# Optimization experiments

Measured on AMD Instinct MI355X. Metric: run time of the kernel, lower is better.

Reference implementation:

```python
import jax, jax.numpy as jnp
import numpy as np

N = 100000
E = 3200000
D_IN = 83
D_HID = 1024
N_CLASSES = 25


def setup_inputs() -> dict:
    key = jax.random.key(0)
    ks = jax.random.split(key, 10)
    feature = jax.random.normal(ks[0], (N, D_IN), dtype=jnp.float32)
    edge_row = jax.random.randint(ks[1], (E,), 0, N, dtype=jnp.int32)
    edge_col = jax.random.randint(ks[2], (E,), 0, N, dtype=jnp.int32)
    adj_val = jax.random.uniform(ks[3], (E,), dtype=jnp.float32)
    # Conv1d(1 -> 4, kernel 5, pad 2): weight [out=4, in=1, k=5]
    conv_w = jax.random.normal(ks[4], (4, 1, 5), dtype=jnp.float32) * 0.2
    conv_b = jnp.zeros((4,), dtype=jnp.float32)
    # GCN weights (kaiming-uniform-like scale), zero biases
    W1 = jax.random.uniform(ks[5], (D_IN, D_HID), dtype=jnp.float32,
                            minval=-1.0, maxval=1.0) * np.sqrt(6.0 / D_IN)
    b1 = jnp.zeros((D_HID,), dtype=jnp.float32)
    W2 = jax.random.uniform(ks[6], (D_HID, N_CLASSES), dtype=jnp.float32,
                            minval=-1.0, maxval=1.0) * np.sqrt(6.0 / D_HID)
    b2 = jnp.zeros((N_CLASSES,), dtype=jnp.float32)
    return {"feature": feature, "conv_w": conv_w, "conv_b": conv_b,
            "W1": W1, "b1": b1, "W2": W2, "b2": b2,
            "adj_val": adj_val, "edge_row": edge_row, "edge_col": edge_col}


def _spmm(vals, row, col, X):
    # sparse(adj) @ X : gather source rows, scale by edge value, scatter-add to dest
    return jax.ops.segment_sum(vals[:, None] * X[col], row, num_segments=N)


def reference(feature, conv_w, conv_b, W1, b1, W2, b2, adj_val, edge_row, edge_col):
    # Conv1d prelude: [N,1,83] -> [N,4,83], sum over channels, relu -> [N,83]
    x = jax.lax.conv_general_dilated(
        feature[:, None, :], conv_w, window_strides=(1,), padding=[(2, 2)],
        dimension_numbers=("NCH", "OIH", "NCH"))
    x = x + conv_b[None, :, None]
    x = jax.nn.relu(jnp.sum(x, axis=1))
    # GCN layer 1: relu(A @ (x W1) + b1)
    h = jax.nn.relu(_spmm(adj_val, edge_row, edge_col, x @ W1) + b1)
    # GCN layer 2: A @ (h W2) + b2
    logits = _spmm(adj_val, edge_row, edge_col, h @ W2) + b2
    return logits
```

## Files before the change

### kernel.cpp

```cpp
#include <hip/hip_runtime.h>

#define NN   100000
#define EE   3200000
#define DIN  83
#define DHID 1024
#define NCLS 25
#define XPAD 96
#define ZPAD 32

#define NBK     391
#define CHUNK   8192

typedef __attribute__((__ext_vector_type__(8))) short sh8;
typedef __attribute__((__ext_vector_type__(4))) float f4_t;

static __device__ __forceinline__ float relu_(float v) { return v > 0.f ? v : 0.f; }

static __device__ __forceinline__ unsigned short f2bf(float f) {
  unsigned int u = __float_as_uint(f);
  unsigned int r = u + 0x7FFFu + ((u >> 16) & 1u);
  return (unsigned short)(r >> 16);
}
static __device__ __forceinline__ float bflo(unsigned int q) {
  return __uint_as_float(q << 16);
}
static __device__ __forceinline__ float bfhi(unsigned int q) {
  return __uint_as_float(q & 0xFFFF0000u);
}

__global__ void conv_relu_k(const float* __restrict__ feature,
                            const float* __restrict__ conv_w,
                            const float* __restrict__ conv_b,
                            unsigned short* __restrict__ x) {
  float ws0 = conv_w[0] + conv_w[5] + conv_w[10] + conv_w[15];
  float ws1 = conv_w[1] + conv_w[6] + conv_w[11] + conv_w[16];
  float ws2 = conv_w[2] + conv_w[7] + conv_w[12] + conv_w[17];
  float ws3 = conv_w[3] + conv_w[8] + conv_w[13] + conv_w[18];
  float ws4 = conv_w[4] + conv_w[9] + conv_w[14] + conv_w[19];
  float bs  = conv_b[0] + conv_b[1] + conv_b[2] + conv_b[3];
  const int total = NN * XPAD;
  for (int idx = blockIdx.x * blockDim.x + threadIdx.x; idx < total;
       idx += gridDim.x * blockDim.x) {
    int n = idx / XPAD;
    int i = idx - n * XPAD;
    unsigned short o = 0;
    if (i < DIN) {
      const float* f = feature + (size_t)n * DIN;
      float acc = bs;
      if (i >= 2)      acc += ws0 * f[i - 2];
      if (i >= 1)      acc += ws1 * f[i - 1];
      acc += ws2 * f[i];
      if (i + 1 < DIN) acc += ws3 * f[i + 1];
      if (i + 2 < DIN) acc += ws4 * f[i + 2];
      o = f2bf(relu_(acc));
    }
    x[idx] = o;
  }
}

__global__ void prep_k(const float* __restrict__ W1, unsigned short* __restrict__ w1t,
                       const float* __restrict__ W2, unsigned short* __restrict__ w2t,
                       int* __restrict__ gbk) {
  int idx = blockIdx.x * blockDim.x + threadIdx.x;
  if (idx < DHID * XPAD) {
    int k = idx / DHID;
    int n = idx - k * DHID;
    float v = (k < DIN) ? W1[k * DHID + n] : 0.f;
    w1t[n * XPAD + k] = f2bf(v);
  }
  if (idx < 32 * DHID) {
    int k = idx / 32;
    int n = idx - k * 32;
    float v = (n < NCLS) ? W2[k * NCLS + n] : 0.f;
    w2t[n * DHID + k] = f2bf(v);
  }
  if (idx < NBK * 16) gbk[idx] = 0;
}


__global__ __launch_bounds__(512) void bucket_hist_k(
    const int* __restrict__ row, int* __restrict__ gbk) {
  __shared__ int cnt[NBK];
  const int tid = threadIdx.x;
  for (int b = tid; b < NBK; b += 512) cnt[b] = 0;
  __syncthreads();
  const int cb = blockIdx.x * CHUNK;
  const int csize = (cb + CHUNK <= EE) ? CHUNK : (EE - cb);
  for (int i = tid; i < csize; i += 512)
    atomicAdd(&cnt[row[cb + i] >> 8], 1);
  __syncthreads();
  for (int b = tid; b < NBK; b += 512)
    if (cnt[b]) atomicAdd(&gbk[b * 16], cnt[b]);
}

__global__ void scan_buckets_k(const int* __restrict__ gbk,
                               int* __restrict__ bbase, int* __restrict__ gcur) {
  __shared__ int sd[512];
  int t = threadIdx.x;
  int v = (t < NBK) ? gbk[t * 16] : 0;
  sd[t] = v;
  __syncthreads();
  for (int off = 1; off < 512; off <<= 1) {
    int add = (t >= off) ? sd[t - off] : 0;
    __syncthreads();
    sd[t] += add;
    __syncthreads();
  }
  if (t < NBK) {
    int excl = sd[t] - v;
    bbase[t] = excl;
    gcur[t * 16] = excl;
  }
  if (t == 0) bbase[NBK] = EE;
}

__global__ __launch_bounds__(256) void partition_k(
    const float* __restrict__ vals, const int* __restrict__ row,
    const int* __restrict__ col, int* __restrict__ gcur,
    int2* __restrict__ tmp) {
  __shared__ int cnt[NBK];
  __shared__ int lcur[NBK];
  const int tid = threadIdx.x;
  const int cb = blockIdx.x * CHUNK;
  const int csize = (cb + CHUNK <= EE) ? CHUNK : (EE - cb);

  for (int b = tid; b < NBK; b += 256) cnt[b] = 0;
  __syncthreads();
  for (int i = tid; i < csize; i += 256)
    atomicAdd(&cnt[row[cb + i] >> 8], 1);
  __syncthreads();
  for (int b = tid; b < NBK; b += 256)
    lcur[b] = cnt[b] ? atomicAdd(&gcur[b * 16], cnt[b]) : 0;
  __syncthreads();
  for (int i = tid; i < csize; i += 256) {
    int r = row[cb + i];
    int pos = atomicAdd(&lcur[r >> 8], 1);
    tmp[pos] = make_int2(col[cb + i] | ((r & 255) << 17),
                         __float_as_int(vals[cb + i]));
  }
}

__global__ __launch_bounds__(512) void fine_scatter2_k(
    const int* __restrict__ bbase, const int2* __restrict__ tmp,
    int2* __restrict__ csr, int* __restrict__ offs, int* __restrict__ counts) {
  __shared__ int cnt[256];
  __shared__ int sd[256];
  __shared__ int lcur[256];
  const int tid = threadIdx.x;
  const int b = blockIdx.x;
  const int r0 = b * 256;
  const int gstart = bbase[b];
  const int nedge = bbase[b + 1] - gstart;
  if (tid < 256) cnt[tid] = 0;
  __syncthreads();
  for (int i = tid; i < nedge; i += 512)
    atomicAdd(&cnt[((unsigned)tmp[gstart + i].x) >> 17], 1);
  __syncthreads();
  int v = 0;
  if (tid < 256) { v = cnt[tid]; sd[tid] = v; }
  __syncthreads();
  for (int off = 1; off < 256; off <<= 1) {
    int add = (tid >= off && tid < 256) ? sd[tid - off] : 0;
    __syncthreads();
    if (tid < 256) sd[tid] += add;
    __syncthreads();
  }
  if (tid < 256) {
    int excl = gstart + sd[tid] - v;
    int r = r0 + tid;
    if (r < NN) {
      offs[r] = excl;
      counts[r] = v;
    }
    lcur[tid] = excl;
  }
  __syncthreads();
  for (int i = tid; i < nedge; i += 512) {
    int2 p = tmp[gstart + i];
    int rl = ((unsigned)p.x) >> 17;
    int pos = atomicAdd(&lcur[rl], 1);
    csr[pos] = make_int2(p.x & 0x1FFFF, p.y);
  }
}

__global__ __launch_bounds__(256) void spmm83_g(
    const int* __restrict__ offs, const int* __restrict__ cnt,
    const int2* __restrict__ csr, const unsigned short* __restrict__ x,
    unsigned short* __restrict__ ax) {
  int wave = (int)((blockIdx.x * blockDim.x + threadIdx.x) >> 6);
  int lane = threadIdx.x & 63;
  if (wave >= NN) return;
  int s = __builtin_amdgcn_readfirstlane(offs[wave]);
  int n = __builtin_amdgcn_readfirstlane(cnt[wave]);
  const bool act = lane < 48;
  const int d2 = lane * 2;
  float a0 = 0.f, a1 = 0.f;
  int i = 0;
  for (; i + 8 <= n; i += 8) {
    int2 p[8];
#pragma unroll
    for (int u = 0; u < 8; ++u) p[u] = csr[s + i + u];
    if (act) {
      unsigned int q[8];
#pragma unroll
      for (int u = 0; u < 8; ++u)
        q[u] = *(const unsigned int*)&x[(size_t)p[u].x * XPAD + d2];
#pragma unroll
      for (int u = 0; u < 8; ++u) {
        float v = __int_as_float(p[u].y);
        a0 += v * bflo(q[u]);
        a1 += v * bfhi(q[u]);
      }
    }
  }
  for (; i < n; ++i) {
    int2 p = csr[s + i];
    if (act) {
      unsigned int q = *(const unsigned int*)&x[(size_t)p.x * XPAD + d2];
      float v = __int_as_float(p.y);
      a0 += v * bflo(q);
      a1 += v * bfhi(q);
    }
  }
  if (act) {
    unsigned int o = (unsigned int)f2bf(a0) | ((unsigned int)f2bf(a1) << 16);
    *(unsigned int*)&ax[(size_t)wave * XPAD + d2] = o;
  }
}

__global__ __launch_bounds__(256) void spmm25_g(
    const int* __restrict__ offs, const int* __restrict__ cnt,
    const int2* __restrict__ csr, const unsigned short* __restrict__ zb,
    const float* __restrict__ b2, float* __restrict__ out) {
  int gw = (int)((blockIdx.x * blockDim.x + threadIdx.x) >> 6);
  int lane = threadIdx.x & 63;
  int sub = lane >> 4;
  int d2 = (lane & 15) * 2;
  int r = gw * 4 + sub;
  if (r >= NN) return;
  int s = offs[r];
  int n = cnt[r];
  float a0 = 0.f, a1 = 0.f;
  int i = 0;
  for (; i + 4 <= n; i += 4) {
    int2 p0 = csr[s + i + 0];
    int2 p1 = csr[s + i + 1];
    int2 p2 = csr[s + i + 2];
    int2 p3 = csr[s + i + 3];
    unsigned int q0 = *(const unsigned int*)&zb[(size_t)p0.x * ZPAD + d2];
    unsigned int q1 = *(const unsigned int*)&zb[(size_t)p1.x * ZPAD + d2];
    unsigned int q2 = *(const unsigned int*)&zb[(size_t)p2.x * ZPAD + d2];
    unsigned int q3 = *(const unsigned int*)&zb[(size_t)p3.x * ZPAD + d2];
    float v0 = __int_as_float(p0.y), v1 = __int_as_float(p1.y);
    float v2 = __int_as_float(p2.y), v3 = __int_as_float(p3.y);
    a0 += v0 * bflo(q0) + v1 * bflo(q1) + v2 * bflo(q2) + v3 * bflo(q3);
    a1 += v0 * bfhi(q0) + v1 * bfhi(q1) + v2 * bfhi(q2) + v3 * bfhi(q3);
  }
  for (; i < n; ++i) {
    int2 p = csr[s + i];
    unsigned int q = *(const unsigned int*)&zb[(size_t)p.x * ZPAD + d2];
    float v = __int_as_float(p.y);
    a0 += v * bflo(q);
    a1 += v * bfhi(q);
  }
  if (d2 < NCLS)     out[(size_t)r * NCLS + d2]     = a0 + b2[d2];
  if (d2 + 1 < NCLS) out[(size_t)r * NCLS + d2 + 1] = a1 + b2[d2 + 1];
}

__global__ __launch_bounds__(256) void fused_mlp_mfma(
    const unsigned short* __restrict__ axg, const unsigned short* __restrict__ w1t,
    const float* __restrict__ b1, const unsigned short* __restrict__ w2t,
    unsigned short* __restrict__ zb) {
  __shared__ __align__(16) unsigned short axs[128 * 104];
  __shared__ __align__(16) unsigned short hs[128 * 136];
  __shared__ float b1s[DHID];
  const int tid = threadIdx.x;
  const int n0 = blockIdx.x * 128;

  for (int idx = tid; idx < 128 * 12; idx += 256) {
    int m = idx / 12;
    int c8 = idx - m * 12;
    int node = n0 + m;
    sh8 v = {0, 0, 0, 0, 0, 0, 0, 0};
    if (node < NN) v = *(const sh8*)&axg[(size_t)node * XPAD + c8 * 8];
    *(sh8*)&axs[m * 104 + c8 * 8] = v;
  }
  for (int i = tid; i < DHID; i += 256) b1s[i] = b1[i];
  __syncthreads();

  const int lane = tid & 63;
  const int w = tid >> 6;
  const int quad = lane >> 4;
  const int tn = lane & 15;
  const int mta = w;
  const int mtb = w + 4;

  sh8 a1[8][3];
#pragma unroll
  for (int mt = 0; mt < 8; ++mt)
#pragma unroll
    for (int kc = 0; kc < 3; ++kc)
      a1[mt][kc] = *(const sh8*)&axs[(mt * 16 + tn) * 104 + kc * 32 + quad * 8];

  f4_t za0 = {0.f, 0.f, 0.f, 0.f}, za1 = {0.f, 0.f, 0.f, 0.f};
  f4_t zb0 = {0.f, 0.f, 0.f, 0.f}, zb1 = {0.f, 0.f, 0.f, 0.f};

  for (int c = 0; c < 8; ++c) {
    const int cb = c * 128;
#pragma unroll
    for (int nti = 0; nti < 2; ++nti) {
      const int nt = w * 2 + nti;
      const int ng = cb + nt * 16 + tn;
      const unsigned short* wr = &w1t[(size_t)ng * XPAD + quad * 8];
      sh8 b0 = *(const sh8*)&wr[0];
      sh8 b1f = *(const sh8*)&wr[32];
      sh8 b2f = *(const sh8*)&wr[64];
      float bias = b1s[ng];
#pragma unroll
      for (int mt = 0; mt < 8; ++mt) {
        f4_t acc = {0.f, 0.f, 0.f, 0.f};
        acc = __builtin_amdgcn_mfma_f32_16x16x32_bf16(a1[mt][0], b0, acc, 0, 0, 0);
        acc = __builtin_amdgcn_mfma_f32_16x16x32_bf16(a1[mt][1], b1f, acc, 0, 0, 0);
        acc = __builtin_amdgcn_mfma_f32_16x16x32_bf16(a1[mt][2], b2f, acc, 0, 0, 0);
#pragma unroll
        for (int r = 0; r < 4; ++r) {
          float v = relu_(acc[r] + bias);
          hs[(mt * 16 + quad * 4 + r) * 136 + nt * 16 + tn] = f2bf(v);
        }
      }
    }
    __syncthreads();
#pragma unroll
    for (int kc = 0; kc < 4; ++kc) {
      sh8 bl = *(const sh8*)&w2t[(size_t)tn * DHID + cb + kc * 32 + quad * 8];
      sh8 bh = *(const sh8*)&w2t[(size_t)(16 + tn) * DHID + cb + kc * 32 + quad * 8];
      sh8 aa = *(const sh8*)&hs[(mta * 16 + tn) * 136 + kc * 32 + quad * 8];
      za0 = __builtin_amdgcn_mfma_f32_16x16x32_bf16(aa, bl, za0, 0, 0, 0);
      za1 = __builtin_amdgcn_mfma_f32_16x16x32_bf16(aa, bh, za1, 0, 0, 0);
      sh8 ab = *(const sh8*)&hs[(mtb * 16 + tn) * 136 + kc * 32 + quad * 8];
      zb0 = __builtin_amdgcn_mfma_f32_16x16x32_bf16(ab, bl, zb0, 0, 0, 0);
      zb1 = __builtin_amdgcn_mfma_f32_16x16x32_bf16(ab, bh, zb1, 0, 0, 0);
    }
    __syncthreads();
  }

#pragma unroll
  for (int r = 0; r < 4; ++r) {
    int na = n0 + mta * 16 + quad * 4 + r;
    if (na < NN) {
      zb[(size_t)na * ZPAD + tn]      = f2bf(za0[r]);
      zb[(size_t)na * ZPAD + 16 + tn] = f2bf(za1[r]);
    }
    int nb = n0 + mtb * 16 + quad * 4 + r;
    if (nb < NN) {
      zb[(size_t)nb * ZPAD + tn]      = f2bf(zb0[r]);
      zb[(size_t)nb * ZPAD + 16 + tn] = f2bf(zb1[r]);
    }
  }
}

extern "C" void kernel_launch(void* const* d_in, const int* in_sizes, int n_in,
                              void* d_out, int out_size, void* d_ws, size_t ws_size,
                              hipStream_t stream) {
  const float* feature = (const float*)d_in[0];
  const float* conv_w  = (const float*)d_in[1];
  const float* conv_b  = (const float*)d_in[2];
  const float* W1      = (const float*)d_in[3];
  const float* b1      = (const float*)d_in[4];
  const float* W2      = (const float*)d_in[5];
  const float* b2      = (const float*)d_in[6];
  const float* adj     = (const float*)d_in[7];
  const int*   erow    = (const int*)d_in[8];
  const int*   ecol    = (const int*)d_in[9];
  float* out = (float*)d_out;

  char* B = (char*)d_ws;
  size_t o = 0;
  auto alloc = [&](size_t bytes, size_t align) -> void* {
    o = (o + align - 1) & ~(align - 1);
    void* p = B + o;
    o += bytes;
    return p;
  };
  unsigned short* x    = (unsigned short*)alloc((size_t)NN * XPAD * 2, 16);
  unsigned short* ax   = (unsigned short*)alloc((size_t)NN * XPAD * 2, 16);
  unsigned short* zb   = (unsigned short*)alloc((size_t)NN * ZPAD * 2, 16);
  int*   counts  = (int*)alloc((size_t)NN * 4, 16);
  int*   offs    = (int*)alloc((size_t)NN * 4, 16);
  int*   gcur    = (int*)alloc((size_t)NBK * 16 * 4, 64);
  int*   gbk     = (int*)alloc((size_t)NBK * 16 * 4, 64);
  int*   bbase   = (int*)alloc((size_t)(NBK + 1) * 4, 16);
  unsigned short* w1t = (unsigned short*)alloc((size_t)DHID * XPAD * 2, 16);
  unsigned short* w2t = (unsigned short*)alloc((size_t)32 * DHID * 2, 16);
  int2*  tmp     = (int2*)alloc((size_t)EE * 8, 16);
  int2*  csr     = (int2*)alloc((size_t)EE * 8, 16);

  conv_relu_k<<<8192, 256, 0, stream>>>(feature, conv_w, conv_b, x);
  prep_k<<<(DHID * XPAD + 255) / 256, 256, 0, stream>>>(W1, w1t, W2, w2t, gbk);
  bucket_hist_k<<<(EE + CHUNK - 1) / CHUNK, 512, 0, stream>>>(erow, gbk);
  scan_buckets_k<<<1, 512, 0, stream>>>(gbk, bbase, gcur);
  partition_k<<<(EE + CHUNK - 1) / CHUNK, 256, 0, stream>>>(adj, erow, ecol, gcur, tmp);
  fine_scatter2_k<<<NBK, 512, 0, stream>>>(bbase, tmp, csr, offs, counts);
  spmm83_g<<<(NN + 3) / 4, 256, 0, stream>>>(offs, counts, csr, x, ax);
  fused_mlp_mfma<<<(NN + 127) / 128, 256, 0, stream>>>(ax, w1t, b1, w2t, zb);
  spmm25_g<<<(NN + 15) / 16, 256, 0, stream>>>(offs, counts, csr, zb, b2, out);
}
```

Before: 483.7 us.

## Sort edges by source-column phase within row groups to improve gather locality

```diff
diff --git a/kernel.cpp b/kernel.cpp
--- a/kernel.cpp
+++ b/kernel.cpp
@@ -10,6 +10,11 @@
 
 #define NBK     391
 #define CHUNK   8192
+
+#define CB      13
+#define NP      13
+#define NKEY    (NP * 256)
+#define NWAVE   (NN / 16)
 
 typedef __attribute__((__ext_vector_type__(8))) short sh8;
 typedef __attribute__((__ext_vector_type__(4))) float f4_t;
@@ -140,131 +145,199 @@
   }
 }
 
-__global__ __launch_bounds__(512) void fine_scatter2_k(
+__global__ __launch_bounds__(512) void fine_scatter3_k(
     const int* __restrict__ bbase, const int2* __restrict__ tmp,
-    int2* __restrict__ csr, int* __restrict__ offs, int* __restrict__ counts) {
-  __shared__ int cnt[256];
-  __shared__ int sd[256];
-  __shared__ int lcur[256];
+    int2* __restrict__ csr2, int* __restrict__ off3) {
+  __shared__ int cnt[3584];
+  __shared__ int lcur[3584];
+  __shared__ int sd[512];
   const int tid = threadIdx.x;
   const int b = blockIdx.x;
-  const int r0 = b * 256;
   const int gstart = bbase[b];
   const int nedge = bbase[b + 1] - gstart;
-  if (tid < 256) cnt[tid] = 0;
-  __syncthreads();
-  for (int i = tid; i < nedge; i += 512)
-    atomicAdd(&cnt[((unsigned)tmp[gstart + i].x) >> 17], 1);
-  __syncthreads();
-  int v = 0;
-  if (tid < 256) { v = cnt[tid]; sd[tid] = v; }
-  __syncthreads();
-  for (int off = 1; off < 256; off <<= 1) {
-    int add = (tid >= off && tid < 256) ? sd[tid - off] : 0;
-    __syncthreads();
-    if (tid < 256) sd[tid] += add;
-    __syncthreads();
-  }
-  if (tid < 256) {
-    int excl = gstart + sd[tid] - v;
-    int r = r0 + tid;
-    if (r < NN) {
-      offs[r] = excl;
-      counts[r] = v;
-    }
-    lcur[tid] = excl;
-  }
+  for (int k = tid; k < 3584; k += 512) cnt[k] = 0;
+  __syncthreads();
+  for (int i = tid; i < nedge; i += 512) {
+    int px = tmp[gstart + i].x;
+    int key = ((px & 0x1FFFF) >> CB) * 256 + (int)(((unsigned)px) >> 17);
+    atomicAdd(&cnt[key], 1);
+  }
+  __syncthreads();
+  int v[7];
+  int run = 0;
+#pragma unroll
+  for (int j = 0; j < 7; ++j) { v[j] = cnt[tid * 7 + j]; run += v[j]; }
+  sd[tid] = run;
+  __syncthreads();
+  for (int off = 1; off < 512; off <<= 1) {
+    int add = (tid >= off) ? sd[tid - off] : 0;
+    __syncthreads();
+    sd[tid] += add;
+    __syncthreads();
+  }
+  int base = gstart + sd[tid] - run;
+#pragma unroll
+  for (int j = 0; j < 7; ++j) { cnt[tid * 7 + j] = base; base += v[j]; }
+  __syncthreads();
+  for (int k = tid; k < 3584; k += 512) lcur[k] = cnt[k];
+  for (int k = tid; k < NKEY; k += 512) off3[b * NKEY + k] = cnt[k];
+  if (b == NBK - 1 && tid == 0) off3[NBK * NKEY] = EE;
   __syncthreads();
   for (int i = tid; i < nedge; i += 512) {
     int2 p = tmp[gstart + i];
-    int rl = ((unsigned)p.x) >> 17;
-    int pos = atomicAdd(&lcur[rl], 1);
-    csr[pos] = make_int2(p.x & 0x1FFFF, p.y);
-  }
-}
-
-__global__ __launch_bounds__(256) void spmm83_g(
-    const int* __restrict__ offs, const int* __restrict__ cnt,
-    const int2* __restrict__ csr, const unsigned short* __restrict__ x,
-    unsigned short* __restrict__ ax) {
-  int wave = (int)((blockIdx.x * blockDim.x + threadIdx.x) >> 6);
-  int lane = threadIdx.x & 63;
-  if (wave >= NN) return;
-  int s = __builtin_amdgcn_readfirstlane(offs[wave]);
-  int n = __builtin_amdgcn_readfirstlane(cnt[wave]);
+    int rloc = (int)(((unsigned)p.x) >> 17);
+    int key = ((p.x & 0x1FFFF) >> CB) * 256 + rloc;
+    int pos = atomicAdd(&lcur[key], 1);
+    csr2[pos] = make_int2((p.x & 0x1FFFF) | ((rloc & 15) << 17), p.y);
+  }
+}
+
+#define FLUSH16(SCUR, C0, C1)                              \
+  switch (SCUR) {                                          \
+    case 0:  a0[0]  += (C0); a1[0]  += (C1); break;        \
+    case 1:  a0[1]  += (C0); a1[1]  += (C1); break;        \
+    case 2:  a0[2]  += (C0); a1[2]  += (C1); break;        \
+    case 3:  a0[3]  += (C0); a1[3]  += (C1); break;        \
+    case 4:  a0[4]  += (C0); a1[4]  += (C1); break;        \
+    case 5:  a0[5]  += (C0); a1[5]  += (C1); break;        \
+    case 6:  a0[6]  += (C0); a1[6]  += (C1); break;        \
+    case 7:  a0[7]  += (C0); a1[7]  += (C1); break;        \
+    case 8:  a0[8]  += (C0); a1[8]  += (C1); break;        \
+    case 9:  a0[9]  += (C0); a1[9]  += (C1); break;        \
+    case 10: a0[10] += (C0); a1[10] += (C1); break;        \
+    case 11: a0[11] += (C0); a1[11] += (C1); break;        \
+    case 12: a0[12] += (C0); a1[12] += (C1); break;        \
+    case 13: a0[13] += (C0); a1[13] += (C1); break;        \
+    case 14: a0[14] += (C0); a1[14] += (C1); break;        \
+    case 15: a0[15] += (C0); a1[15] += (C1); break;        \
+    default: break;                                        \
+  }
+
+__global__ __launch_bounds__(512, 8) void spmm83_p(
+    const int* __restrict__ off3, const int2* __restrict__ csr2,
+    const unsigned short* __restrict__ x, unsigned short* __restrict__ ax) {
+  const int gw = (int)((blockIdx.x * 512 + threadIdx.x) >> 6);
+  const int lane = threadIdx.x & 63;
+  if (gw >= NWAVE) return;
+  const int b = gw >> 4;
+  const int g0 = (gw & 15) << 4;
   const bool act = lane < 48;
   const int d2 = lane * 2;
-  float a0 = 0.f, a1 = 0.f;
-  int i = 0;
-  for (; i + 8 <= n; i += 8) {
-    int2 p[8];
-#pragma unroll
-    for (int u = 0; u < 8; ++u) p[u] = csr[s + i + u];
-    if (act) {
-      unsigned int q[8];
-#pragma unroll
-      for (int u = 0; u < 8; ++u)
-        q[u] = *(const unsigned int*)&x[(size_t)p[u].x * XPAD + d2];
-#pragma unroll
-      for (int u = 0; u < 8; ++u) {
-        float v = __int_as_float(p[u].y);
-        a0 += v * bflo(q[u]);
-        a1 += v * bfhi(q[u]);
-      }
-    }
-  }
-  for (; i < n; ++i) {
-    int2 p = csr[s + i];
-    if (act) {
-      unsigned int q = *(const unsigned int*)&x[(size_t)p.x * XPAD + d2];
-      float v = __int_as_float(p.y);
-      a0 += v * bflo(q);
-      a1 += v * bfhi(q);
-    }
-  }
+  float a0[16], a1[16];
+#pragma unroll
+  for (int k = 0; k < 16; ++k) { a0[k] = 0.f; a1[k] = 0.f; }
+
+  for (int p = 0; p < NP; ++p) {
+    const int kb = b * NKEY + p * 256 + g0;
+    const int s = __builtin_amdgcn_readfirstlane(off3[kb]);
+    const int e = __builtin_amdgcn_readfirstlane(off3[kb + 16]);
+    int scur = 0;
+    float c0 = 0.f, c1 = 0.f;
+    int i = s;
+    for (; i + 4 <= e; i += 4) {
+      int2 p4[4];
+#pragma unroll
+      for (int u = 0; u < 4; ++u) p4[u] = csr2[i + u];
+      unsigned q[4];
+      if (act) {
+#pragma unroll
+        for (int u = 0; u < 4; ++u)
+          q[u] = *(const unsigned*)&x[(size_t)(p4[u].x & 0x1FFFF) * XPAD + d2];
+      }
+#pragma unroll
+      for (int u = 0; u < 4; ++u) {
+        int srl = __builtin_amdgcn_readfirstlane((int)(((unsigned)p4[u].x) >> 17));
+        if (srl != scur) {
+          FLUSH16(scur, c0, c1);
+          scur = srl; c0 = 0.f; c1 = 0.f;
+        }
+        float v = __int_as_float(p4[u].y);
+        c0 += v * bflo(q[u]);
+        c1 += v * bfhi(q[u]);
+      }
+    }
+    for (; i < e; ++i) {
+      int2 pe = csr2[i];
+      unsigned q = 0;
+      if (act) q = *(const unsigned*)&x[(size_t)(pe.x & 0x1FFFF) * XPAD + d2];
+      int srl = __builtin_amdgcn_readfirstlane((int)(((unsigned)pe.x) >> 17));
+      if (srl != scur) {
+        FLUSH16(scur, c0, c1);
+        scur = srl; c0 = 0.f; c1 = 0.f;
+      }
+      float v = __int_as_float(pe.y);
+      c0 += v * bflo(q);
+      c1 += v * bfhi(q);
+    }
+    FLUSH16(scur, c0, c1);
+  }
+
   if (act) {
-    unsigned int o = (unsigned int)f2bf(a0) | ((unsigned int)f2bf(a1) << 16);
-    *(unsigned int*)&ax[(size_t)wave * XPAD + d2] = o;
-  }
-}
-
-__global__ __launch_bounds__(256) void spmm25_g(
-    const int* __restrict__ offs, const int* __restrict__ cnt,
-    const int2* __restrict__ csr, const unsigned short* __restrict__ zb,
-    const float* __restrict__ b2, float* __restrict__ out) {
-  int gw = (int)((blockIdx.x * blockDim.x + threadIdx.x) >> 6);
-  int lane = threadIdx.x & 63;
-  int sub = lane >> 4;
-  int d2 = (lane & 15) * 2;
-  int r = gw * 4 + sub;
-  if (r >= NN) return;
-  int s = offs[r];
-  int n = cnt[r];
-  float a0 = 0.f, a1 = 0.f;
-  int i = 0;
-  for (; i + 4 <= n; i += 4) {
-    int2 p0 = csr[s + i + 0];
-    int2 p1 = csr[s + i + 1];
-    int2 p2 = csr[s + i + 2];
-    int2 p3 = csr[s + i + 3];
-    unsigned int q0 = *(const unsigned int*)&zb[(size_t)p0.x * ZPAD + d2];
-    unsigned int q1 = *(const unsigned int*)&zb[(size_t)p1.x * ZPAD + d2];
-    unsigned int q2 = *(const unsigned int*)&zb[(size_t)p2.x * ZPAD + d2];
-    unsigned int q3 = *(const unsigned int*)&zb[(size_t)p3.x * ZPAD + d2];
-    float v0 = __int_as_float(p0.y), v1 = __int_as_float(p1.y);
-    float v2 = __int_as_float(p2.y), v3 = __int_as_float(p3.y);
-    a0 += v0 * bflo(q0) + v1 * bflo(q1) + v2 * bflo(q2) + v3 * bflo(q3);
-    a1 += v0 * bfhi(q0) + v1 * bfhi(q1) + v2 * bfhi(q2) + v3 * bfhi(q3);
-  }
-  for (; i < n; ++i) {
-    int2 p = csr[s + i];
-    unsigned int q = *(const unsigned int*)&zb[(size_t)p.x * ZPAD + d2];
-    float v = __int_as_float(p.y);
-    a0 += v * bflo(q);
-    a1 += v * bfhi(q);
-  }
-  if (d2 < NCLS)     out[(size_t)r * NCLS + d2]     = a0 + b2[d2];
-  if (d2 + 1 < NCLS) out[(size_t)r * NCLS + d2 + 1] = a1 + b2[d2 + 1];
+    const int r0 = gw << 4;
+#pragma unroll
+    for (int k = 0; k < 16; ++k) {
+      unsigned o = (unsigned)f2bf(a0[k]) | ((unsigned)f2bf(a1[k]) << 16);
+      *(unsigned*)&ax[(size_t)(r0 + k) * XPAD + d2] = o;
+    }
+  }
+}
+
+__global__ __launch_bounds__(512, 8) void spmm25_p(
+    const int* __restrict__ off3, const int2* __restrict__ csr2,
+    const unsigned short* __restrict__ zbt, const float* __restrict__ b2,
+    float* __restrict__ out) {
+  const int gw = (int)((blockIdx.x * 512 + threadIdx.x) >> 6);
+  const int lane = threadIdx.x & 63;
+  if (gw >= NWAVE) return;
+  const int b = gw >> 4;
+  const int g0 = (gw & 15) << 4;
+  const int grp = lane >> 4;
+  const int d2 = (lane & 15) * 2;
+  float acc0[4], acc1[4];
+#pragma unroll
+  for (int s = 0; s < 4; ++s) { acc0[s] = 0.f; acc1[s] = 0.f; }
+
+  for (int p = 0; p < NP; ++p) {
+    const int kb = b * NKEY + p * 256 + g0;
+#pragma unroll
+    for (int s = 0; s < 4; ++s) {
+      const int st = __builtin_amdgcn_readfirstlane(off3[kb + s * 4]);
+      const int en = __builtin_amdgcn_readfirstlane(off3[kb + s * 4 + 4]);
+      const int myrl = s * 4 + grp;
+      float t0 = acc0[s], t1 = acc1[s];
+      int i = st;
+      for (; i + 4 <= en; i += 4) {
+        int2 p4[4];
+#pragma unroll
+        for (int u = 0; u < 4; ++u) p4[u] = csr2[i + u];
+#pragma unroll
+        for (int u = 0; u < 4; ++u) {
+          unsigned q = *(const unsigned*)&zbt[(size_t)(p4[u].x & 0x1FFFF) * ZPAD + d2];
+          int rl = (int)(((unsigned)p4[u].x) >> 17);
+          float v = (rl == myrl) ? __int_as_float(p4[u].y) : 0.f;
+          t0 += v * bflo(q);
+          t1 += v * bfhi(q);
+        }
+      }
+      for (; i < en; ++i) {
+        int2 pe = csr2[i];
+        unsigned q = *(const unsigned*)&zbt[(size_t)(pe.x & 0x1FFFF) * ZPAD + d2];
+        int rl = (int)(((unsigned)pe.x) >> 17);
+        float v = (rl == myrl) ? __int_as_float(pe.y) : 0.f;
+        t0 += v * bflo(q);
+        t1 += v * bfhi(q);
+      }
+      acc0[s] = t0; acc1[s] = t1;
+    }
+  }
+
+  const int r0 = gw << 4;
+#pragma unroll
+  for (int s = 0; s < 4; ++s) {
+    int r = r0 + s * 4 + grp;
+    if (d2 < NCLS)     out[(size_t)r * NCLS + d2]     = acc0[s] + b2[d2];
+    if (d2 + 1 < NCLS) out[(size_t)r * NCLS + d2 + 1] = acc1[s] + b2[d2 + 1];
+  }
 }
 
 __global__ __launch_bounds__(256) void fused_mlp_mfma(
@@ -385,23 +458,22 @@
   unsigned short* x    = (unsigned short*)alloc((size_t)NN * XPAD * 2, 16);
   unsigned short* ax   = (unsigned short*)alloc((size_t)NN * XPAD * 2, 16);
   unsigned short* zb   = (unsigned short*)alloc((size_t)NN * ZPAD * 2, 16);
-  int*   counts  = (int*)alloc((size_t)NN * 4, 16);
-  int*   offs    = (int*)alloc((size_t)NN * 4, 16);
   int*   gcur    = (int*)alloc((size_t)NBK * 16 * 4, 64);
   int*   gbk     = (int*)alloc((size_t)NBK * 16 * 4, 64);
   int*   bbase   = (int*)alloc((size_t)(NBK + 1) * 4, 16);
+  int*   off3    = (int*)alloc(((size_t)NBK * NKEY + 1) * 4, 16);
   unsigned short* w1t = (unsigned short*)alloc((size_t)DHID * XPAD * 2, 16);
   unsigned short* w2t = (unsigned short*)alloc((size_t)32 * DHID * 2, 16);
   int2*  tmp     = (int2*)alloc((size_t)EE * 8, 16);
-  int2*  csr     = (int2*)alloc((size_t)EE * 8, 16);
+  int2*  csr2    = (int2*)alloc((size_t)EE * 8, 16);
 
   conv_relu_k<<<8192, 256, 0, stream>>>(feature, conv_w, conv_b, x);
   prep_k<<<(DHID * XPAD + 255) / 256, 256, 0, stream>>>(W1, w1t, W2, w2t, gbk);
   bucket_hist_k<<<(EE + CHUNK - 1) / CHUNK, 512, 0, stream>>>(erow, gbk);
   scan_buckets_k<<<1, 512, 0, stream>>>(gbk, bbase, gcur);
   partition_k<<<(EE + CHUNK - 1) / CHUNK, 256, 0, stream>>>(adj, erow, ecol, gcur, tmp);
-  fine_scatter2_k<<<NBK, 512, 0, stream>>>(bbase, tmp, csr, offs, counts);
-  spmm83_g<<<(NN + 3) / 4, 256, 0, stream>>>(offs, counts, csr, x, ax);
+  fine_scatter3_k<<<NBK, 512, 0, stream>>>(bbase, tmp, csr2, off3);
+  spmm83_p<<<(NWAVE * 64 + 511) / 512, 512, 0, stream>>>(off3, csr2, x, ax);
   fused_mlp_mfma<<<(NN + 127) / 128, 256, 0, stream>>>(ax, w1t, b1, w2t, zb);
-  spmm25_g<<<(NN + 15) / 16, 256, 0, stream>>>(offs, counts, csr, zb, b2, out);
-}
+  spmm25_p<<<(NWAVE * 64 + 511) / 512, 512, 0, stream>>>(off3, csr2, zb, b2, out);
+}
```

Result: slower. 1.806 ms (+273.3%).

## Sort edges by source-column phase within row buckets to localize layer-1 gathers

Applied to the files above, without the earlier changes.

```diff
diff --git a/kernel.cpp b/kernel.cpp
--- a/kernel.cpp
+++ b/kernel.cpp
@@ -8,8 +8,13 @@
 #define XPAD 96
 #define ZPAD 32
 
-#define NBK     391
+#define NBK     782
 #define CHUNK   8192
+
+#define CB      13
+#define NP      13
+#define NKEY    (NP * 128)
+#define PADK    2048
 
 typedef __attribute__((__ext_vector_type__(8))) short sh8;
 typedef __attribute__((__ext_vector_type__(4))) float f4_t;
@@ -87,7 +92,7 @@
   const int cb = blockIdx.x * CHUNK;
   const int csize = (cb + CHUNK <= EE) ? CHUNK : (EE - cb);
   for (int i = tid; i < csize; i += 512)
-    atomicAdd(&cnt[row[cb + i] >> 8], 1);
+    atomicAdd(&cnt[row[cb + i] >> 7], 1);
   __syncthreads();
   for (int b = tid; b < NBK; b += 512)
     if (cnt[b]) atomicAdd(&gbk[b * 16], cnt[b]);
@@ -95,12 +100,12 @@
 
 __global__ void scan_buckets_k(const int* __restrict__ gbk,
                                int* __restrict__ bbase, int* __restrict__ gcur) {
-  __shared__ int sd[512];
+  __shared__ int sd[1024];
   int t = threadIdx.x;
   int v = (t < NBK) ? gbk[t * 16] : 0;
   sd[t] = v;
   __syncthreads();
-  for (int off = 1; off < 512; off <<= 1) {
+  for (int off = 1; off < 1024; off <<= 1) {
     int add = (t >= off) ? sd[t - off] : 0;
     __syncthreads();
     sd[t] += add;
@@ -127,104 +132,148 @@
   for (int b = tid; b < NBK; b += 256) cnt[b] = 0;
   __syncthreads();
   for (int i = tid; i < csize; i += 256)
-    atomicAdd(&cnt[row[cb + i] >> 8], 1);
+    atomicAdd(&cnt[row[cb + i] >> 7], 1);
   __syncthreads();
   for (int b = tid; b < NBK; b += 256)
     lcur[b] = cnt[b] ? atomicAdd(&gcur[b * 16], cnt[b]) : 0;
   __syncthreads();
   for (int i = tid; i < csize; i += 256) {
     int r = row[cb + i];
-    int pos = atomicAdd(&lcur[r >> 8], 1);
-    tmp[pos] = make_int2(col[cb + i] | ((r & 255) << 17),
+    int pos = atomicAdd(&lcur[r >> 7], 1);
+    tmp[pos] = make_int2(col[cb + i] | ((r & 127) << 17),
                          __float_as_int(vals[cb + i]));
   }
 }
 
-__global__ __launch_bounds__(512) void fine_scatter2_k(
+__global__ __launch_bounds__(512) void fine_scatter4_k(
     const int* __restrict__ bbase, const int2* __restrict__ tmp,
-    int2* __restrict__ csr, int* __restrict__ offs, int* __restrict__ counts) {
-  __shared__ int cnt[256];
-  __shared__ int sd[256];
-  __shared__ int lcur[256];
+    int2* __restrict__ csr2, int* __restrict__ off3) {
+  __shared__ int cnt[PADK];
+  __shared__ int lcur[PADK];
+  __shared__ int sd[512];
   const int tid = threadIdx.x;
   const int b = blockIdx.x;
-  const int r0 = b * 256;
   const int gstart = bbase[b];
   const int nedge = bbase[b + 1] - gstart;
-  if (tid < 256) cnt[tid] = 0;
-  __syncthreads();
-  for (int i = tid; i < nedge; i += 512)
-    atomicAdd(&cnt[((unsigned)tmp[gstart + i].x) >> 17], 1);
-  __syncthreads();
-  int v = 0;
-  if (tid < 256) { v = cnt[tid]; sd[tid] = v; }
-  __syncthreads();
-  for (int off = 1; off < 256; off <<= 1) {
-    int add = (tid >= off && tid < 256) ? sd[tid - off] : 0;
-    __syncthreads();
-    if (tid < 256) sd[tid] += add;
-    __syncthreads();
-  }
-  if (tid < 256) {
-    int excl = gstart + sd[tid] - v;
-    int r = r0 + tid;
-    if (r < NN) {
-      offs[r] = excl;
-      counts[r] = v;
-    }
-    lcur[tid] = excl;
-  }
+  for (int k = tid; k < PADK; k += 512) cnt[k] = 0;
+  __syncthreads();
+  for (int i = tid; i < nedge; i += 512) {
+    int px = tmp[gstart + i].x;
+    int key = ((px & 0x1FFFF) >> CB) * 128 + (int)(((unsigned)px) >> 17);
+    atomicAdd(&cnt[key], 1);
+  }
+  __syncthreads();
+  int v[4];
+  int run = 0;
+#pragma unroll
+  for (int j = 0; j < 4; ++j) { v[j] = cnt[tid * 4 + j]; run += v[j]; }
+  sd[tid] = run;
+  __syncthreads();
+  for (int off = 1; off < 512; off <<= 1) {
+    int add = (tid >= off) ? sd[tid - off] : 0;
+    __syncthreads();
+    sd[tid] += add;
+    __syncthreads();
+  }
+  int base = gstart + sd[tid] - run;
+#pragma unroll
+  for (int j = 0; j < 4; ++j) { cnt[tid * 4 + j] = base; base += v[j]; }
+  __syncthreads();
+  for (int k = tid; k < PADK; k += 512) lcur[k] = cnt[k];
+  for (int k = tid; k < NKEY; k += 512) off3[b * NKEY + k] = cnt[k];
+  if (b == NBK - 1 && tid == 0) off3[NBK * NKEY] = EE;
   __syncthreads();
   for (int i = tid; i < nedge; i += 512) {
     int2 p = tmp[gstart + i];
-    int rl = ((unsigned)p.x) >> 17;
+    int key = ((p.x & 0x1FFFF) >> CB) * 128 + (int)(((unsigned)p.x) >> 17);
+    int pos = atomicAdd(&lcur[key], 1);
+    csr2[pos] = p;
+  }
+}
+
+__global__ __launch_bounds__(512) void fine_row_k(
+    const int* __restrict__ bbase, const int2* __restrict__ csr2,
+    int2* __restrict__ csr, int* __restrict__ offs, int* __restrict__ counts) {
+  __shared__ int cnt[128];
+  __shared__ int sd[128];
+  __shared__ int lcur[128];
+  const int tid = threadIdx.x;
+  const int b = blockIdx.x;
+  const int gstart = bbase[b];
+  const int nedge = bbase[b + 1] - gstart;
+  if (tid < 128) cnt[tid] = 0;
+  __syncthreads();
+  for (int i = tid; i < nedge; i += 512)
+    atomicAdd(&cnt[((unsigned)csr2[gstart + i].x) >> 17], 1);
+  __syncthreads();
+  int v = 0;
+  if (tid < 128) { v = cnt[tid]; sd[tid] = v; }
+  __syncthreads();
+  for (int off = 1; off < 128; off <<= 1) {
+    int add = (tid >= off && tid < 128) ? sd[tid - off] : 0;
+    __syncthreads();
+    if (tid < 128) sd[tid] += add;
+    __syncthreads();
+  }
+  if (tid < 128) {
+    int excl = gstart + sd[tid] - v;
+    int r = (b << 7) + tid;
+    if (r < NN) { offs[r] = excl; counts[r] = v; }
+    lcur[tid] = excl;
+  }
+  __syncthreads();
+  for (int i = tid; i < nedge; i += 512) {
+    int2 p = csr2[gstart + i];
+    int rl = (int)(((unsigned)p.x) >> 17);
     int pos = atomicAdd(&lcur[rl], 1);
     csr[pos] = make_int2(p.x & 0x1FFFF, p.y);
   }
 }
 
-__global__ __launch_bounds__(256) void spmm83_g(
-    const int* __restrict__ offs, const int* __restrict__ cnt,
-    const int2* __restrict__ csr, const unsigned short* __restrict__ x,
-    unsigned short* __restrict__ ax) {
-  int wave = (int)((blockIdx.x * blockDim.x + threadIdx.x) >> 6);
-  int lane = threadIdx.x & 63;
-  if (wave >= NN) return;
-  int s = __builtin_amdgcn_readfirstlane(offs[wave]);
-  int n = __builtin_amdgcn_readfirstlane(cnt[wave]);
+__global__ __launch_bounds__(512, 6) void spmm83_ph(
+    const int* __restrict__ off3, const int2* __restrict__ csr2,
+    const unsigned short* __restrict__ x, unsigned short* __restrict__ ax) {
+  const int b = blockIdx.x;
+  const int w = threadIdx.x >> 6;
+  const int lane = threadIdx.x & 63;
   const bool act = lane < 48;
-  const int d2 = lane * 2;
-  float a0 = 0.f, a1 = 0.f;
-  int i = 0;
-  for (; i + 8 <= n; i += 8) {
-    int2 p[8];
-#pragma unroll
-    for (int u = 0; u < 8; ++u) p[u] = csr[s + i + u];
-    if (act) {
-      unsigned int q[8];
-#pragma unroll
-      for (int u = 0; u < 8; ++u)
-        q[u] = *(const unsigned int*)&x[(size_t)p[u].x * XPAD + d2];
-#pragma unroll
-      for (int u = 0; u < 8; ++u) {
-        float v = __int_as_float(p[u].y);
-        a0 += v * bflo(q[u]);
-        a1 += v * bfhi(q[u]);
+  const int d2 = act ? lane * 2 : 0;
+  float c0[16], c1[16];
+#pragma unroll
+  for (int k = 0; k < 16; ++k) { c0[k] = 0.f; c1[k] = 0.f; }
+
+  const int idx17 = (lane < 17 ? lane : 16) + w * 16;
+  int bv = off3[b * NKEY + idx17];
+  for (int p = 0; p < NP; ++p) {
+    int bvn = 0;
+    if (p + 1 < NP) bvn = off3[b * NKEY + (p + 1) * 128 + idx17];
+#pragma unroll
+    for (int k = 0; k < 16; ++k) {
+      int s = __builtin_amdgcn_readlane(bv, k);
+      int e = __builtin_amdgcn_readlane(bv, k + 1);
+      float t0 = c0[k], t1 = c1[k];
+      for (int i = s; i < e; ++i) {
+        int2 pe = csr2[i];
+        unsigned q = *(const unsigned*)&x[(size_t)(pe.x & 0x1FFFF) * XPAD + d2];
+        float v = __int_as_float(pe.y);
+        t0 += v * bflo(q);
+        t1 += v * bfhi(q);
       }
-    }
-  }
-  for (; i < n; ++i) {
-    int2 p = csr[s + i];
-    if (act) {
-      unsigned int q = *(const unsigned int*)&x[(size_t)p.x * XPAD + d2];
-      float v = __int_as_float(p.y);
-      a0 += v * bflo(q);
-      a1 += v * bfhi(q);
-    }
-  }
+      c0[k] = t0; c1[k] = t1;
+    }
+    bv = bvn;
+  }
+
   if (act) {
-    unsigned int o = (unsigned int)f2bf(a0) | ((unsigned int)f2bf(a1) << 16);
-    *(unsigned int*)&ax[(size_t)wave * XPAD + d2] = o;
+    const int r0 = (b << 7) + (w << 4);
+#pragma unroll
+    for (int k = 0; k < 16; ++k) {
+      int r = r0 + k;
+      if (r < NN) {
+        unsigned o = (unsigned)f2bf(c0[k]) | ((unsigned)f2bf(c1[k]) << 16);
+        *(unsigned*)&ax[(size_t)r * XPAD + d2] = o;
+      }
+    }
   }
 }
 
@@ -390,18 +439,21 @@
   int*   gcur    = (int*)alloc((size_t)NBK * 16 * 4, 64);
   int*   gbk     = (int*)alloc((size_t)NBK * 16 * 4, 64);
   int*   bbase   = (int*)alloc((size_t)(NBK + 1) * 4, 16);
+  int*   off3    = (int*)alloc(((size_t)NBK * NKEY + 1) * 4, 16);
   unsigned short* w1t = (unsigned short*)alloc((size_t)DHID * XPAD * 2, 16);
   unsigned short* w2t = (unsigned short*)alloc((size_t)32 * DHID * 2, 16);
   int2*  tmp     = (int2*)alloc((size_t)EE * 8, 16);
-  int2*  csr     = (int2*)alloc((size_t)EE * 8, 16);
+  int2*  csr2    = (int2*)alloc((size_t)EE * 8, 16);
+  int2*  csr     = tmp;
 
   conv_relu_k<<<8192, 256, 0, stream>>>(feature, conv_w, conv_b, x);
   prep_k<<<(DHID * XPAD + 255) / 256, 256, 0, stream>>>(W1, w1t, W2, w2t, gbk);
   bucket_hist_k<<<(EE + CHUNK - 1) / CHUNK, 512, 0, stream>>>(erow, gbk);
-  scan_buckets_k<<<1, 512, 0, stream>>>(gbk, bbase, gcur);
+  scan_buckets_k<<<1, 1024, 0, stream>>>(gbk, bbase, gcur);
   partition_k<<<(EE + CHUNK - 1) / CHUNK, 256, 0, stream>>>(adj, erow, ecol, gcur, tmp);
-  fine_scatter2_k<<<NBK, 512, 0, stream>>>(bbase, tmp, csr, offs, counts);
-  spmm83_g<<<(NN + 3) / 4, 256, 0, stream>>>(offs, counts, csr, x, ax);
+  fine_scatter4_k<<<NBK, 512, 0, stream>>>(bbase, tmp, csr2, off3);
+  fine_row_k<<<NBK, 512, 0, stream>>>(bbase, csr2, csr, offs, counts);
+  spmm83_ph<<<NBK, 512, 0, stream>>>(off3, csr2, x, ax);
   fused_mlp_mfma<<<(NN + 127) / 128, 256, 0, stream>>>(ax, w1t, b1, w2t, zb);
   spmm25_g<<<(NN + 15) / 16, 256, 0, stream>>>(offs, counts, csr, zb, b2, out);
 }
```

Result: slower. 619.9 us (+28.2%).
